# Performance work log

Measured on AMD Instinct MI355X. Metric: run time of the kernel, lower is better.

## Reference

```python
import jax, jax.numpy as jnp
import numpy as np

TOP_K = 16
NUM_HEADS = 1
EPS = 1e-8  # torch F.cosine_similarity eps


def setup_inputs() -> dict:
    key = jax.random.key(0)
    ks = jax.random.split(key, 8)
    B, N, Dk, Dv = 64, 8192, 256, 256
    return {
        "query": jax.random.normal(ks[0], (B, Dk), jnp.float32),
        "key_memory": jax.random.normal(ks[1], (B, N, Dk), jnp.float32),
        "value_memory": jax.random.normal(ks[2], (B, N, Dv), jnp.float32),
        "iteration": jax.random.randint(ks[3], (B, 1), 0, N),
        "in_proj_w": jax.random.normal(ks[4], (3 * Dv, Dv), jnp.float32) * 0.06,
        "in_proj_b": jnp.zeros((3 * Dv,), jnp.float32),
        "out_proj_w": jax.random.normal(ks[5], (Dv, Dv), jnp.float32) * 0.06,
        "out_proj_b": jnp.zeros((Dv,), jnp.float32),
    }


def _mha(x, in_w, in_b, out_w, out_b):
    # torch nn.MultiheadAttention (batch_first, qkv same embed dim) self-attention
    B, T, E = x.shape
    H = NUM_HEADS
    hd = E // H
    qkv = x @ in_w.T + in_b                      # [B,T,3E]
    q, k, v = jnp.split(qkv, 3, axis=-1)

    def heads(t):
        return t.reshape(B, T, H, hd).transpose(0, 2, 1, 3)  # [B,H,T,hd]

    q, k, v = heads(q), heads(k), heads(v)
    scale = jnp.asarray(1.0 / np.sqrt(hd), x.dtype)
    attn = jax.nn.softmax(jnp.einsum('bhqd,bhkd->bhqk', q, k) * scale, axis=-1)
    o = jnp.einsum('bhqk,bhkd->bhqd', attn, v).transpose(0, 2, 1, 3).reshape(B, T, E)
    return o @ out_w.T + out_b


def reference(query, key_memory, value_memory, iteration,
              in_proj_w, in_proj_b, out_proj_w, out_proj_b):
    B, N, Dv = value_memory.shape
    # memory validity mask: item n is valid iff n <= iteration[b]
    mem_idx = jnp.arange(N)[None, :]                                   # [1,N]
    mask = (mem_idx <= iteration).astype(key_memory.dtype)[..., None]  # [B,N,1]
    km = key_memory * mask
    vm = value_memory * mask

    # masked cosine similarity between each memory key and the query
    num = jnp.einsum('bnd,bd->bn', km, query)                          # [B,N]
    denom = jnp.maximum(
        jnp.linalg.norm(km, axis=-1) * jnp.linalg.norm(query, axis=-1, keepdims=True),
        EPS)
    sim = num / denom                                                  # [B,N]

    topk_sim, topk_idx = jax.lax.top_k(sim, TOP_K)                     # [B,K]
    topk_vm = jnp.take_along_axis(vm, topk_idx[:, :, None], axis=1)    # [B,K,Dv]

    wv = jax.nn.softmax(topk_sim, axis=-1)[..., None]                  # [B,K,1]
    nrv = wv * topk_vm                                                 # [B,K,Dv]

    nrv = _mha(nrv, in_proj_w, in_proj_b, out_proj_w, out_proj_b)      # [B,K,Dv]

    # rows with iteration == 0 are left as zeros (scatter of computed rows)
    not_first = (iteration.reshape(-1) > 0).astype(nrv.dtype)[:, None, None]
    nrv = nrv * not_first
    return nrv.sum(axis=1)                                             # [B,Dv]
```

## Files before the change

### kernel.cpp

```cpp
#include <hip/hip_runtime.h>
#include <hip/hip_bf16.h>
#include <math.h>

#define B_   64
#define N_   8192
#define D_   256
#define K_   16
#define EPS_ 1e-8f
#define NEG_ -3.4e38f

static const size_t CANDV_OFF = 0;
static const size_t CANDI_OFF = 131072;

__global__ void __launch_bounds__(256)
simtopk_kernel(const float* __restrict__ q, const float* __restrict__ km,
               const int* __restrict__ iter,
               float* __restrict__ cand_v, int* __restrict__ cand_i) {
    int tid  = threadIdx.x;
    int w    = tid >> 6, lane = tid & 63;
    int g    = lane >> 4, p = lane & 15;
    int item = (blockIdx.x << 2) + w;
    int b    = item >> 7;
    int r0   = (item & 127) << 6;
    int it   = iter[b];
    size_t cbase = (size_t)item * K_;

    if (r0 > it) {
        if (lane < K_) { cand_v[cbase + lane] = 0.f; cand_i[cbase + lane] = r0 + lane; }
        return;
    }

    float4 q4[4];
    #pragma unroll
    for (int kk = 0; kk < 4; kk++)
        q4[kk] = *(const float4*)(q + (size_t)b * D_ + kk * 64 + p * 4);
    float qq = 0.f;
    #pragma unroll
    for (int kk = 0; kk < 4; kk++)
        qq += q4[kk].x*q4[kk].x + q4[kk].y*q4[kk].y + q4[kk].z*q4[kk].z + q4[kk].w*q4[kk].w;
    #pragma unroll
    for (int off = 8; off; off >>= 1) qq += __shfl_xor(qq, off);
    float qn = sqrtf(qq);

    float keepv = 0.f;
    const float* kmb = km + (size_t)b * N_ * D_;
    for (int t = 0; t < 8; t++) {
        int ra = r0 + (t << 3) + (g << 1);
        int rb = ra + 1;
        const float* pa = kmb + (size_t)min(ra, it) * D_;
        const float* pb = kmb + (size_t)min(rb, it) * D_;
        float4 ka0 = *(const float4*)(pa +   0 + p * 4);
        float4 ka1 = *(const float4*)(pa +  64 + p * 4);
        float4 ka2 = *(const float4*)(pa + 128 + p * 4);
        float4 ka3 = *(const float4*)(pa + 192 + p * 4);
        float4 kb0 = *(const float4*)(pb +   0 + p * 4);
        float4 kb1 = *(const float4*)(pb +  64 + p * 4);
        float4 kb2 = *(const float4*)(pb + 128 + p * 4);
        float4 kb3 = *(const float4*)(pb + 192 + p * 4);
        float dota = ka0.x*q4[0].x + ka0.y*q4[0].y + ka0.z*q4[0].z + ka0.w*q4[0].w
                   + ka1.x*q4[1].x + ka1.y*q4[1].y + ka1.z*q4[1].z + ka1.w*q4[1].w
                   + ka2.x*q4[2].x + ka2.y*q4[2].y + ka2.z*q4[2].z + ka2.w*q4[2].w
                   + ka3.x*q4[3].x + ka3.y*q4[3].y + ka3.z*q4[3].z + ka3.w*q4[3].w;
        float sqa  = ka0.x*ka0.x + ka0.y*ka0.y + ka0.z*ka0.z + ka0.w*ka0.w
                   + ka1.x*ka1.x + ka1.y*ka1.y + ka1.z*ka1.z + ka1.w*ka1.w
                   + ka2.x*ka2.x + ka2.y*ka2.y + ka2.z*ka2.z + ka2.w*ka2.w
                   + ka3.x*ka3.x + ka3.y*ka3.y + ka3.z*ka3.z + ka3.w*ka3.w;
        float dotb = kb0.x*q4[0].x + kb0.y*q4[0].y + kb0.z*q4[0].z + kb0.w*q4[0].w
                   + kb1.x*q4[1].x + kb1.y*q4[1].y + kb1.z*q4[1].z + kb1.w*q4[1].w
                   + kb2.x*q4[2].x + kb2.y*q4[2].y + kb2.z*q4[2].z + kb2.w*q4[2].w
                   + kb3.x*q4[3].x + kb3.y*q4[3].y + kb3.z*q4[3].z + kb3.w*q4[3].w;
        float sqb  = kb0.x*kb0.x + kb0.y*kb0.y + kb0.z*kb0.z + kb0.w*kb0.w
                   + kb1.x*kb1.x + kb1.y*kb1.y + kb1.z*kb1.z + kb1.w*kb1.w
                   + kb2.x*kb2.x + kb2.y*kb2.y + kb2.z*kb2.z + kb2.w*kb2.w
                   + kb3.x*kb3.x + kb3.y*kb3.y + kb3.z*kb3.z + kb3.w*kb3.w;
        #pragma unroll
        for (int off = 8; off; off >>= 1) {
            dota += __shfl_xor(dota, off);
            sqa  += __shfl_xor(sqa,  off);
            dotb += __shfl_xor(dotb, off);
            sqb  += __shfl_xor(sqb,  off);
        }
        float sa = (ra <= it) ? dota / fmaxf(sqrtf(sqa) * qn, EPS_) : 0.f;
        float sb = (rb <= it) ? dotb / fmaxf(sqrtf(sqb) * qn, EPS_) : 0.f;
        keepv = (p == 2 * t)     ? sa : keepv;
        keepv = (p == 2 * t + 1) ? sb : keepv;
    }
    int keepi = r0 + ((p >> 1) << 3) + (g << 1) + (p & 1);

    #pragma unroll
    for (int k = 2; k <= 64; k <<= 1) {
        #pragma unroll
        for (int j = k >> 1; j > 0; j >>= 1) {
            float pv = __shfl_xor(keepv, j);
            int   pi = __shfl_xor(keepi, j);
            bool up         = ((lane & k) == 0);
            bool is_lower   = ((lane & j) == 0);
            bool mine_first = (keepv > pv) || (keepv == pv && keepi < pi);
            bool take_mine  = ((is_lower == up) == mine_first);
            if (!take_mine) { keepv = pv; keepi = pi; }
        }
    }
    if (lane < K_) { cand_v[cbase + lane] = keepv; cand_i[cbase + lane] = keepi; }
}

__global__ void __launch_bounds__(768)
tail_kernel(const float* __restrict__ cand_v, const int* __restrict__ cand_i,
            const float* __restrict__ vm, const int* __restrict__ iter,
            const float* __restrict__ inw, const float* __restrict__ inb,
            const float* __restrict__ ow, const float* __restrict__ ob,
            float* __restrict__ out) {
    int b = blockIdx.x;
    int tid = threadIdx.x, lane = tid & 63;
    int it = iter[b];
    if (it == 0) {
        if (tid < D_) out[(size_t)b * D_ + tid] = 0.f;
        return;
    }

    __shared__ int   seli[K_];
    __shared__ float scl[K_];
    __shared__ float xs[D_][K_];
    __shared__ float qs[K_][260];
    __shared__ float ks[K_][260];
    __shared__ float vs[K_][260];
    __shared__ float attnS[K_][K_];
    __shared__ float colsum[K_];
    __shared__ float so[D_];

    if (tid < 64) {
        float cv[32]; int ci[32];
        #pragma unroll
        for (int j = 0; j < 32; j++) {
            cv[j] = cand_v[(size_t)b * 2048 + (j << 6) + lane];
            ci[j] = cand_i[(size_t)b * 2048 + (j << 6) + lane];
        }
        float selv[K_]; int selidx[K_];
        for (int sel = 0; sel < K_; sel++) {
            float bv = cv[0]; int bi = ci[0];
            #pragma unroll
            for (int j = 1; j < 32; j++)
                if (cv[j] > bv || (cv[j] == bv && ci[j] < bi)) { bv = cv[j]; bi = ci[j]; }
            #pragma unroll
            for (int off = 32; off; off >>= 1) {
                float ov = __shfl_xor(bv, off);
                int   oi = __shfl_xor(bi, off);
                if (ov > bv || (ov == bv && oi < bi)) { bv = ov; bi = oi; }
            }
            #pragma unroll
            for (int j = 0; j < 32; j++)
                if (ci[j] == bi) cv[j] = NEG_;
            selv[sel] = bv; selidx[sel] = bi;
            if (lane == 0) seli[sel] = bi;
        }
        float m = NEG_;
        #pragma unroll
        for (int jj = 0; jj < K_; jj++) m = fmaxf(m, selv[jj]);
        float ssum = 0.f;
        #pragma unroll
        for (int jj = 0; jj < K_; jj++) ssum += expf(selv[jj] - m);
        if (lane < K_) {
            float wgt = expf(selv[lane] - m) / ssum;
            scl[lane] = (selidx[lane] <= it) ? wgt : 0.f;
        }
    }
    __syncthreads();

    if (tid < D_) {
        #pragma unroll
        for (int kk = 0; kk < K_; kk += 4) {
            float4 px;
            px.x = scl[kk+0] * vm[((size_t)b * N_ + seli[kk+0]) * D_ + tid];
            px.y = scl[kk+1] * vm[((size_t)b * N_ + seli[kk+1]) * D_ + tid];
            px.z = scl[kk+2] * vm[((size_t)b * N_ + seli[kk+2]) * D_ + tid];
            px.w = scl[kk+3] * vm[((size_t)b * N_ + seli[kk+3]) * D_ + tid];
            *(float4*)(&xs[tid][kk]) = px;
        }
    }
    __syncthreads();

    {
        int which = tid >> 8, e = tid & 255;
        float acc[K_];
        #pragma unroll
        for (int k = 0; k < K_; k++) acc[k] = 0.f;
        const float* wrow = inw + (size_t)(which * D_ + e) * D_;
        for (int d = 0; d < D_; d += 4) {
            float4 wv4 = *(const float4*)(wrow + d);
            float wk[4] = {wv4.x, wv4.y, wv4.z, wv4.w};
            #pragma unroll
            for (int dd = 0; dd < 4; dd++) {
                float wgt = wk[dd];
                float4 x0 = *(const float4*)(&xs[d + dd][0]);
                float4 x1 = *(const float4*)(&xs[d + dd][4]);
                float4 x2 = *(const float4*)(&xs[d + dd][8]);
                float4 x3 = *(const float4*)(&xs[d + dd][12]);
                acc[0]  += x0.x * wgt; acc[1]  += x0.y * wgt; acc[2]  += x0.z * wgt; acc[3]  += x0.w * wgt;
                acc[4]  += x1.x * wgt; acc[5]  += x1.y * wgt; acc[6]  += x1.z * wgt; acc[7]  += x1.w * wgt;
                acc[8]  += x2.x * wgt; acc[9]  += x2.y * wgt; acc[10] += x2.z * wgt; acc[11] += x2.w * wgt;
                acc[12] += x3.x * wgt; acc[13] += x3.y * wgt; acc[14] += x3.z * wgt; acc[15] += x3.w * wgt;
            }
        }
        float bias = inb[which * D_ + e];
        float* dst = (which == 0) ? &qs[0][0] : (which == 1) ? &ks[0][0] : &vs[0][0];
        #pragma unroll
        for (int k = 0; k < K_; k++)
            dst[k * 260 + e] = acc[k] + bias;
    }
    __syncthreads();

    if (tid < D_) {
        int i = tid >> 4, j = tid & 15;
        float s = 0.f;
        for (int d4 = 0; d4 < 64; d4++) {
            float4 qv = *(const float4*)(&qs[i][d4 * 4]);
            float4 kv = *(const float4*)(&ks[j][d4 * 4]);
            s += qv.x*kv.x + qv.y*kv.y + qv.z*kv.z + qv.w*kv.w;
        }
        attnS[i][j] = s * 0.0625f;
    }
    __syncthreads();
    if (tid < K_) {
        float m = NEG_;
        for (int jj = 0; jj < K_; jj++) m = fmaxf(m, attnS[tid][jj]);
        float ssum = 0.f;
        for (int jj = 0; jj < K_; jj++) ssum += expf(attnS[tid][jj] - m);
        float inv = 1.f / ssum;
        for (int jj = 0; jj < K_; jj++) attnS[tid][jj] = expf(attnS[tid][jj] - m) * inv;
    }
    __syncthreads();
    if (tid < K_) {
        float c = 0.f;
        for (int ii = 0; ii < K_; ii++) c += attnS[ii][tid];
        colsum[tid] = c;
    }
    __syncthreads();
    if (tid < D_) {
        float acc = 0.f;
        #pragma unroll
        for (int jj = 0; jj < K_; jj++) acc += colsum[jj] * vs[jj][tid];
        so[tid] = acc;
    }
    __syncthreads();
    if (tid < D_) {
        float o = 0.f;
        const float* orow = ow + (size_t)tid * D_;
        for (int e = 0; e < D_; e += 4) {
            float4 wv = *(const float4*)(orow + e);
            float4 sv = *(const float4*)(&so[e]);
            o += sv.x*wv.x + sv.y*wv.y + sv.z*wv.z + sv.w*wv.w;
        }
        out[(size_t)b * D_ + tid] = o + 16.f * ob[tid];
    }
}

extern "C" void kernel_launch(void* const* d_in, const int* in_sizes, int n_in,
                              void* d_out, int out_size, void* d_ws, size_t ws_size,
                              hipStream_t stream) {
    const float* q   = (const float*)d_in[0];
    const float* km  = (const float*)d_in[1];
    const float* vm  = (const float*)d_in[2];
    const int*   it  = (const int*)  d_in[3];
    const float* inw = (const float*)d_in[4];
    const float* inb = (const float*)d_in[5];
    const float* ow  = (const float*)d_in[6];
    const float* ob  = (const float*)d_in[7];
    float* out = (float*)d_out;

    float* ws     = (float*)d_ws;
    float* cand_v = ws + CANDV_OFF;
    int*   cand_i = (int*)(ws + CANDI_OFF);

    simtopk_kernel<<<dim3(2048), dim3(256), 0, stream>>>(q, km, it, cand_v, cand_i);
    tail_kernel<<<dim3(B_), dim3(768), 0, stream>>>(cand_v, cand_i, vm, it, inw, inb, ow, ob, out);
}
```

Baseline: 131.8 us.

## Compact valid segments into a worklist and run persistent waves over it

Adds a single-block plan kernel that counts the valid 64-row segments per batch row (up to iteration) and writes a compacted worklist. The similarity/top-k kernel now launches a fixed grid of 4096 waves that loop over only the valid segments, then fill placeholder candidates for the invalid ones. This is meant to balance load, since the old grid mapped one wave to each segment and many waves exited immediately. It costs an extra serial kernel launch and a dependent global read of the worklist.

```diff
diff --git a/kernel.cpp b/kernel.cpp
--- a/kernel.cpp
+++ b/kernel.cpp
@@ -6,101 +6,134 @@
 #define N_   8192
 #define D_   256
 #define K_   16
+#define NSEG_ 8192
+#define NWAVE_ 4096
 #define EPS_ 1e-8f
 #define NEG_ -3.4e38f
 
 static const size_t CANDV_OFF = 0;
 static const size_t CANDI_OFF = 131072;
+static const size_t WORK_OFF  = 262144;
+static const size_t VTOT_OFF  = 270336;
+
+__global__ void plan_kernel(const int* __restrict__ iter,
+                            int* __restrict__ worklist, int* __restrict__ vtotal) {
+    __shared__ int nseg[B_];
+    __shared__ int off[B_];
+    int tid = threadIdx.x;
+    if (tid < B_) nseg[tid] = (min(iter[tid], N_ - 1) >> 6) + 1;
+    __syncthreads();
+    if (tid == 0) {
+        int s = 0;
+        for (int b = 0; b < B_; b++) { off[b] = s; s += nseg[b]; }
+        *vtotal = s;
+    }
+    __syncthreads();
+    for (int b = 0; b < B_; b++) {
+        int n = nseg[b], o = off[b];
+        for (int j = tid; j < n; j += 256) worklist[o + j] = (b << 7) | j;
+    }
+}
 
 __global__ void __launch_bounds__(256)
 simtopk_kernel(const float* __restrict__ q, const float* __restrict__ km,
                const int* __restrict__ iter,
+               const int* __restrict__ worklist, const int* __restrict__ vtotal,
                float* __restrict__ cand_v, int* __restrict__ cand_i) {
     int tid  = threadIdx.x;
     int w    = tid >> 6, lane = tid & 63;
     int g    = lane >> 4, p = lane & 15;
-    int item = (blockIdx.x << 2) + w;
-    int b    = item >> 7;
-    int r0   = (item & 127) << 6;
-    int it   = iter[b];
-    size_t cbase = (size_t)item * K_;
-
-    if (r0 > it) {
-        if (lane < K_) { cand_v[cbase + lane] = 0.f; cand_i[cbase + lane] = r0 + lane; }
-        return;
-    }
-
-    float4 q4[4];
-    #pragma unroll
-    for (int kk = 0; kk < 4; kk++)
-        q4[kk] = *(const float4*)(q + (size_t)b * D_ + kk * 64 + p * 4);
-    float qq = 0.f;
-    #pragma unroll
-    for (int kk = 0; kk < 4; kk++)
-        qq += q4[kk].x*q4[kk].x + q4[kk].y*q4[kk].y + q4[kk].z*q4[kk].z + q4[kk].w*q4[kk].w;
-    #pragma unroll
-    for (int off = 8; off; off >>= 1) qq += __shfl_xor(qq, off);
-    float qn = sqrtf(qq);
-
-    float keepv = 0.f;
-    const float* kmb = km + (size_t)b * N_ * D_;
-    for (int t = 0; t < 8; t++) {
-        int ra = r0 + (t << 3) + (g << 1);
-        int rb = ra + 1;
-        const float* pa = kmb + (size_t)min(ra, it) * D_;
-        const float* pb = kmb + (size_t)min(rb, it) * D_;
-        float4 ka0 = *(const float4*)(pa +   0 + p * 4);
-        float4 ka1 = *(const float4*)(pa +  64 + p * 4);
-        float4 ka2 = *(const float4*)(pa + 128 + p * 4);
-        float4 ka3 = *(const float4*)(pa + 192 + p * 4);
-        float4 kb0 = *(const float4*)(pb +   0 + p * 4);
-        float4 kb1 = *(const float4*)(pb +  64 + p * 4);
-        float4 kb2 = *(const float4*)(pb + 128 + p * 4);
-        float4 kb3 = *(const float4*)(pb + 192 + p * 4);
-        float dota = ka0.x*q4[0].x + ka0.y*q4[0].y + ka0.z*q4[0].z + ka0.w*q4[0].w
-                   + ka1.x*q4[1].x + ka1.y*q4[1].y + ka1.z*q4[1].z + ka1.w*q4[1].w
-                   + ka2.x*q4[2].x + ka2.y*q4[2].y + ka2.z*q4[2].z + ka2.w*q4[2].w
-                   + ka3.x*q4[3].x + ka3.y*q4[3].y + ka3.z*q4[3].z + ka3.w*q4[3].w;
-        float sqa  = ka0.x*ka0.x + ka0.y*ka0.y + ka0.z*ka0.z + ka0.w*ka0.w
-                   + ka1.x*ka1.x + ka1.y*ka1.y + ka1.z*ka1.z + ka1.w*ka1.w
-                   + ka2.x*ka2.x + ka2.y*ka2.y + ka2.z*ka2.z + ka2.w*ka2.w
-                   + ka3.x*ka3.x + ka3.y*ka3.y + ka3.z*ka3.z + ka3.w*ka3.w;
-        float dotb = kb0.x*q4[0].x + kb0.y*q4[0].y + kb0.z*q4[0].z + kb0.w*q4[0].w
-                   + kb1.x*q4[1].x + kb1.y*q4[1].y + kb1.z*q4[1].z + kb1.w*q4[1].w
-                   + kb2.x*q4[2].x + kb2.y*q4[2].y + kb2.z*q4[2].z + kb2.w*q4[2].w
-                   + kb3.x*q4[3].x + kb3.y*q4[3].y + kb3.z*q4[3].z + kb3.w*q4[3].w;
-        float sqb  = kb0.x*kb0.x + kb0.y*kb0.y + kb0.z*kb0.z + kb0.w*kb0.w
-                   + kb1.x*kb1.x + kb1.y*kb1.y + kb1.z*kb1.z + kb1.w*kb1.w
-                   + kb2.x*kb2.x + kb2.y*kb2.y + kb2.z*kb2.z + kb2.w*kb2.w
-                   + kb3.x*kb3.x + kb3.y*kb3.y + kb3.z*kb3.z + kb3.w*kb3.w;
-        #pragma unroll
-        for (int off = 8; off; off >>= 1) {
-            dota += __shfl_xor(dota, off);
-            sqa  += __shfl_xor(sqa,  off);
-            dotb += __shfl_xor(dotb, off);
-            sqb  += __shfl_xor(sqb,  off);
-        }
-        float sa = (ra <= it) ? dota / fmaxf(sqrtf(sqa) * qn, EPS_) : 0.f;
-        float sb = (rb <= it) ? dotb / fmaxf(sqrtf(sqb) * qn, EPS_) : 0.f;
-        keepv = (p == 2 * t)     ? sa : keepv;
-        keepv = (p == 2 * t + 1) ? sb : keepv;
-    }
-    int keepi = r0 + ((p >> 1) << 3) + (g << 1) + (p & 1);
-
-    #pragma unroll
-    for (int k = 2; k <= 64; k <<= 1) {
-        #pragma unroll
-        for (int j = k >> 1; j > 0; j >>= 1) {
-            float pv = __shfl_xor(keepv, j);
-            int   pi = __shfl_xor(keepi, j);
-            bool up         = ((lane & k) == 0);
-            bool is_lower   = ((lane & j) == 0);
-            bool mine_first = (keepv > pv) || (keepv == pv && keepi < pi);
-            bool take_mine  = ((is_lower == up) == mine_first);
-            if (!take_mine) { keepv = pv; keepi = pi; }
-        }
-    }
-    if (lane < K_) { cand_v[cbase + lane] = keepv; cand_i[cbase + lane] = keepi; }
+    int wave_id = (blockIdx.x << 2) + w;
+    int V = *vtotal;
+
+    for (int v = wave_id; v < V; v += NWAVE_) {
+        int seg = worklist[v];
+        int b   = seg >> 7;
+        int r0  = (seg & 127) << 6;
+        int it  = iter[b];
+        size_t cbase = (size_t)seg * K_;
+
+        float4 q4[4];
+        #pragma unroll
+        for (int kk = 0; kk < 4; kk++)
+            q4[kk] = *(const float4*)(q + (size_t)b * D_ + kk * 64 + p * 4);
+        float qq = 0.f;
+        #pragma unroll
+        for (int kk = 0; kk < 4; kk++)
+            qq += q4[kk].x*q4[kk].x + q4[kk].y*q4[kk].y + q4[kk].z*q4[kk].z + q4[kk].w*q4[kk].w;
+        #pragma unroll
+        for (int off = 8; off; off >>= 1) qq += __shfl_xor(qq, off);
+        float qn = sqrtf(qq);
+
+        float keepv = 0.f;
+        const float* kmb = km + (size_t)b * N_ * D_;
+        for (int t = 0; t < 8; t++) {
+            int ra = r0 + (t << 3) + (g << 1);
+            int rb = ra + 1;
+            const float* pa = kmb + (size_t)min(ra, it) * D_;
+            const float* pb = kmb + (size_t)min(rb, it) * D_;
+            float4 ka0 = *(const float4*)(pa +   0 + p * 4);
+            float4 ka1 = *(const float4*)(pa +  64 + p * 4);
+            float4 ka2 = *(const float4*)(pa + 128 + p * 4);
+            float4 ka3 = *(const float4*)(pa + 192 + p * 4);
+            float4 kb0 = *(const float4*)(pb +   0 + p * 4);
+            float4 kb1 = *(const float4*)(pb +  64 + p * 4);
+            float4 kb2 = *(const float4*)(pb + 128 + p * 4);
+            float4 kb3 = *(const float4*)(pb + 192 + p * 4);
+            float dota = ka0.x*q4[0].x + ka0.y*q4[0].y + ka0.z*q4[0].z + ka0.w*q4[0].w
+                       + ka1.x*q4[1].x + ka1.y*q4[1].y + ka1.z*q4[1].z + ka1.w*q4[1].w
+                       + ka2.x*q4[2].x + ka2.y*q4[2].y + ka2.z*q4[2].z + ka2.w*q4[2].w
+                       + ka3.x*q4[3].x + ka3.y*q4[3].y + ka3.z*q4[3].z + ka3.w*q4[3].w;
+            float sqa  = ka0.x*ka0.x + ka0.y*ka0.y + ka0.z*ka0.z + ka0.w*ka0.w
+                       + ka1.x*ka1.x + ka1.y*ka1.y + ka1.z*ka1.z + ka1.w*ka1.w
+                       + ka2.x*ka2.x + ka2.y*ka2.y + ka2.z*ka2.z + ka2.w*ka2.w
+                       + ka3.x*ka3.x + ka3.y*ka3.y + ka3.z*ka3.z + ka3.w*ka3.w;
+            float dotb = kb0.x*q4[0].x + kb0.y*q4[0].y + kb0.z*q4[0].z + kb0.w*q4[0].w
+                       + kb1.x*q4[1].x + kb1.y*q4[1].y + kb1.z*q4[1].z + kb1.w*q4[1].w
+                       + kb2.x*q4[2].x + kb2.y*q4[2].y + kb2.z*q4[2].z + kb2.w*q4[2].w
+                       + kb3.x*q4[3].x + kb3.y*q4[3].y + kb3.z*q4[3].z + kb3.w*q4[3].w;
+            float sqb  = kb0.x*kb0.x + kb0.y*kb0.y + kb0.z*kb0.z + kb0.w*kb0.w
+                       + kb1.x*kb1.x + kb1.y*kb1.y + kb1.z*kb1.z + kb1.w*kb1.w
+                       + kb2.x*kb2.x + kb2.y*kb2.y + kb2.z*kb2.z + kb2.w*kb2.w
+                       + kb3.x*kb3.x + kb3.y*kb3.y + kb3.z*kb3.z + kb3.w*kb3.w;
+            #pragma unroll
+            for (int off = 8; off; off >>= 1) {
+                dota += __shfl_xor(dota, off);
+                sqa  += __shfl_xor(sqa,  off);
+                dotb += __shfl_xor(dotb, off);
+                sqb  += __shfl_xor(sqb,  off);
+            }
+            float sa = (ra <= it) ? dota / fmaxf(sqrtf(sqa) * qn, EPS_) : 0.f;
+            float sb = (rb <= it) ? dotb / fmaxf(sqrtf(sqb) * qn, EPS_) : 0.f;
+            keepv = (p == 2 * t)     ? sa : keepv;
+            keepv = (p == 2 * t + 1) ? sb : keepv;
+        }
+        int keepi = r0 + ((p >> 1) << 3) + (g << 1) + (p & 1);
+
+        #pragma unroll
+        for (int k = 2; k <= 64; k <<= 1) {
+            #pragma unroll
+            for (int j2 = k >> 1; j2 > 0; j2 >>= 1) {
+                float pv = __shfl_xor(keepv, j2);
+                int   pi = __shfl_xor(keepi, j2);
+                bool up         = ((lane & k) == 0);
+                bool is_lower   = ((lane & j2) == 0);
+                bool mine_first = (keepv > pv) || (keepv == pv && keepi < pi);
+                bool take_mine  = ((is_lower == up) == mine_first);
+                if (!take_mine) { keepv = pv; keepi = pi; }
+            }
+        }
+        if (lane < K_) { cand_v[cbase + lane] = keepv; cand_i[cbase + lane] = keepi; }
+    }
+
+    for (int s = wave_id; s < NSEG_; s += NWAVE_) {
+        int b  = s >> 7;
+        int r0 = (s & 127) << 6;
+        if (r0 > iter[b] && lane < K_) {
+            cand_v[(size_t)s * K_ + lane] = 0.f;
+            cand_i[(size_t)s * K_ + lane] = r0 + lane;
+        }
+    }
 }
 
 __global__ void __launch_bounds__(768)
@@ -266,10 +299,13 @@
     const float* ob  = (const float*)d_in[7];
     float* out = (float*)d_out;
 
-    float* ws     = (float*)d_ws;
-    float* cand_v = ws + CANDV_OFF;
-    int*   cand_i = (int*)(ws + CANDI_OFF);
-
-    simtopk_kernel<<<dim3(2048), dim3(256), 0, stream>>>(q, km, it, cand_v, cand_i);
+    float* ws       = (float*)d_ws;
+    float* cand_v   = ws + CANDV_OFF;
+    int*   cand_i   = (int*)(ws + CANDI_OFF);
+    int*   worklist = (int*)(ws + WORK_OFF);
+    int*   vtotal   = (int*)(ws + VTOT_OFF);
+
+    plan_kernel<<<dim3(1), dim3(256), 0, stream>>>(it, worklist, vtotal);
+    simtopk_kernel<<<dim3(1024), dim3(256), 0, stream>>>(q, km, it, worklist, vtotal, cand_v, cand_i);
     tail_kernel<<<dim3(B_), dim3(768), 0, stream>>>(cand_v, cand_i, vm, it, inw, inb, ow, ob, out);
 }
```

New measurement: 137.9 us. +4.7%, slower.
